# Kernel optimization log

Measured on AMD Instinct MI355X. Metric: run time of the kernel, lower is better.

## Reference

```python
import jax, jax.numpy as jnp
import numpy as np

Q_R = jnp.array([-1.0 / np.sqrt(2.0), 1.0 / np.sqrt(2.0)], dtype=jnp.float32)
N_U, N_H, N_MLP, N_CONV, N_Q = 8, 12, 16, 2, 2


def setup_inputs() -> dict:
    B, n = 16, 1024
    key = jax.random.key(0)
    ks = jax.random.split(key, 24)
    lin_w = lambda k, o, i: (jax.random.normal(k, (o, i), jnp.float32) * 0.1)
    lin_b = lambda k, o: (jax.random.normal(k, (o,), jnp.float32) * 0.1)
    inp = {
        "y": jax.random.normal(ks[0], (B, n), jnp.float32),
        "H": jax.random.normal(ks[1], (B, n, n), jnp.float32),
        "r": jax.random.normal(ks[2], (B, n), jnp.float32),
        "nu_r": jax.random.uniform(ks[3], (B, n), jnp.float32),
        "adj": (jax.random.uniform(ks[4], (B, n, n)) < 0.05).astype(jnp.float32),
        # W1: Linear(2, n_u) plus extra bias b1
        "W1_w": lin_w(ks[5], N_U, 2), "W1_b": lin_b(ks[6], N_U),
        "b1": jnp.zeros((N_U,), jnp.float32),
        # msg_mlp: Linear(3*n_u, n_mlp_hidden) -> ReLU -> Linear(n_mlp_hidden, n_u)
        "Wm1_w": lin_w(ks[7], N_MLP, 3 * N_U), "Wm1_b": lin_b(ks[8], N_MLP),
        "Wm2_w": lin_w(ks[9], N_U, N_MLP), "Wm2_b": lin_b(ks[10], N_U),
        # GRUCell(n_u + 2, n_h); gate order: r, z, n
        "gru_w_ih": lin_w(ks[11], 3 * N_H, N_U + 2), "gru_w_hh": lin_w(ks[12], 3 * N_H, N_H),
        "gru_b_ih": lin_b(ks[13], 3 * N_H), "gru_b_hh": lin_b(ks[14], 3 * N_H),
        # W2: Linear(n_h, n_u) plus extra bias b2
        "W2_w": lin_w(ks[15], N_U, N_H), "W2_b": lin_b(ks[16], N_U),
        "b2": jnp.zeros((N_U,), jnp.float32),
        # readout: Linear(n_u, n_mlp_hidden) -> ReLU -> Linear(n_mlp_hidden, N_Q)
        "Wr1_w": lin_w(ks[17], N_MLP, N_U), "Wr1_b": lin_b(ks[18], N_MLP),
        "Wr2_w": lin_w(ks[19], N_Q, N_MLP), "Wr2_b": lin_b(ks[20], N_Q),
    }
    return inp


def reference(y, H, r, nu_r, adj, W1_w, W1_b, b1, Wm1_w, Wm1_b, Wm2_w, Wm2_b,
              gru_w_ih, gru_w_hh, gru_b_ih, gru_b_hh, W2_w, W2_b, b2,
              Wr1_w, Wr1_b, Wr2_w, Wr2_b):
    B, n = y.shape
    yh = jnp.einsum('bi,bij->bj', y, H)          # (B,n)
    hh = jnp.sum(H * H, axis=1)                  # (B,n), column norms
    feat = jnp.stack([yh, hh], axis=-1)          # (B,n,2)
    u = feat @ W1_w.T + W1_b + b1                # (B,n,n_u)
    G = jnp.einsum('bki,bkj->bij', H, H)         # H^T H, (B,n,n)
    a_i = jnp.stack([r, jnp.maximum(nu_r, 1e-10)], axis=-1)  # (B,n,2)

    # masked-sum aggregation, fused (same math as expand+cat+mask+sum):
    #   agg = [u_i * deg_i, sum_j adj_ij u_j, (sum_j adj_ij G_ij) * 1_{n_u}]
    deg = jnp.sum(adj, axis=2)                   # (B,n)
    eg = jnp.sum(adj * G, axis=2)                # (B,n)
    eg_part = jnp.repeat(eg[..., None], N_U, axis=-1)  # (B,n,n_u)

    s = jnp.zeros((B, n, N_H), dtype=y.dtype)
    for _ in range(N_CONV):
        agg = jnp.concatenate([
            u * deg[..., None],
            jnp.einsum('bij,bjd->bid', adj, u),
            eg_part,
        ], axis=-1)                              # (B,n,3*n_u)
        m = jax.nn.relu(agg @ Wm1_w.T + Wm1_b) @ Wm2_w.T + Wm2_b  # (B,n,n_u)
        x = jnp.concatenate([m, a_i], axis=-1)   # (B,n,n_u+2)
        gx = x @ gru_w_ih.T + gru_b_ih
        gh = s @ gru_w_hh.T + gru_b_hh
        xr, xz, xn = jnp.split(gx, 3, axis=-1)
        hr, hz, hn = jnp.split(gh, 3, axis=-1)
        rg = jax.nn.sigmoid(xr + hr)
        zg = jax.nn.sigmoid(xz + hz)
        ng = jnp.tanh(xn + rg * hn)
        s = (1.0 - zg) * ng + zg * s             # (B,n,n_h)
        u = s @ W2_w.T + W2_b + b2               # (B,n,n_u)

    logits = jax.nn.relu(u @ Wr1_w.T + Wr1_b) @ Wr2_w.T + Wr2_b  # (B,n,N_Q)
    p = jax.nn.softmax(logits, axis=-1)
    x_hat = jnp.sum(p * Q_R, axis=-1)            # (B,n)
    nu_x = jnp.sum(p * (Q_R - x_hat[..., None]) ** 2, axis=-1)
    nu_x = jnp.maximum(nu_x, 1e-10)
    return (x_hat, nu_x)
```

## Files before the change

kernel.cpp:

```cpp
#include <hip/hip_runtime.h>

#define NB 16
#define NN 1024
#define NBN (NB * NN)
#define MAXN 128
#define NU 8
#define NH 12
#define NMLP 16
#define KC 16
#define NCHUNK (NN / KC)

#define QSW(j, c) (((j) << 4) + ((((c) ^ (((j) >> 2) & 3)) & 3) << 2))

__global__ __launch_bounds__(256) void k_build_idx(
    const float* __restrict__ adj, unsigned short* __restrict__ idxT,
    int* __restrict__ cnt, float* __restrict__ deg,
    float* __restrict__ eg, float* __restrict__ yhh) {
  const int row = blockIdx.x * 4 + (threadIdx.x >> 6);
  const int lane = threadIdx.x & 63;
  const float4* arow = (const float4*)(adj + (size_t)row * NN);
  float4 v[4];
#pragma unroll
  for (int rep = 0; rep < 4; ++rep) v[rep] = arow[rep * 64 + lane];
  const unsigned long long ltmask = (1ull << lane) - 1ull;
  int base = 0;
#pragma unroll
  for (int rep = 0; rep < 4; ++rep) {
    float c[4] = {v[rep].x, v[rep].y, v[rep].z, v[rep].w};
#pragma unroll
    for (int cc = 0; cc < 4; ++cc) {
      bool nz = (c[cc] != 0.0f);
      unsigned long long m = __ballot(nz);
      if (nz) {
        int p = base + __popcll(m & ltmask);
        if (p < MAXN)
          idxT[(size_t)p * NBN + row] = (unsigned short)(rep * 256 + lane * 4 + cc);
      }
      base += __popcll(m);
    }
  }
  if (lane == 0) {
    cnt[row] = base < MAXN ? base : MAXN;
    deg[row] = (float)base;
    eg[row] = 0.f; yhh[2 * row] = 0.f; yhh[2 * row + 1] = 0.f;
  }
}

__global__ __launch_bounds__(512) void k_eg(
    const float* __restrict__ H, const float* __restrict__ y,
    const unsigned short* __restrict__ idxT, const int* __restrict__ cnt,
    float* __restrict__ eg, float* __restrict__ yhh) {
  __shared__ float hsT[NN * KC];
  const int b = blockIdx.x >> 6;
  const int k0 = (blockIdx.x & 63) * KC;
  const int tid = threadIdx.x;
  const float* Hb = H + ((size_t)b * NN + k0) * NN;

  for (int j0 = tid; j0 < NN; j0 += 512) {
    float hv[KC];
#pragma unroll
    for (int k = 0; k < KC; ++k) hv[k] = Hb[(size_t)k * NN + j0];
#pragma unroll
    for (int c = 0; c < 4; ++c)
      *(float4*)&hsT[QSW(j0, c)] = ((const float4*)hv)[c];
  }
  __syncthreads();

  {
    float yv[KC];
#pragma unroll
    for (int k = 0; k < KC; ++k) yv[k] = y[b * NN + k0 + k];
    for (int j = tid; j < NN; j += 512) {
      float hv[KC];
#pragma unroll
      for (int c = 0; c < 4; ++c)
        ((float4*)hv)[c] = *(const float4*)&hsT[QSW(j, c)];
      float py = 0.f, ph = 0.f;
#pragma unroll
      for (int k = 0; k < KC; ++k) { py += yv[k] * hv[k]; ph += hv[k] * hv[k]; }
      atomicAdd(&yhh[(b * NN + j) * 2], py);
      atomicAdd(&yhh[(b * NN + j) * 2 + 1], ph);
    }
  }

  for (int rep = 0; rep < 2; ++rep) {
    const int i = rep * 512 + tid;
    const int node = b * NN + i;
    const int nnz = cnt[node];
    float hi[KC];
#pragma unroll
    for (int c = 0; c < 4; ++c)
      ((float4*)hi)[c] = *(const float4*)&hsT[QSW(i, c)];
    float a0 = 0.f, a1 = 0.f, a2 = 0.f, a3 = 0.f;
#pragma unroll 2
    for (int t = 0; t < nnz; ++t) {
      const int j = (int)idxT[(size_t)t * NBN + node];
      float hj[KC];
#pragma unroll
      for (int c = 0; c < 4; ++c)
        ((float4*)hj)[c] = *(const float4*)&hsT[QSW(j, c)];
#pragma unroll
      for (int k = 0; k < 4; ++k) {
        a0 += hi[k] * hj[k];
        a1 += hi[4 + k] * hj[4 + k];
        a2 += hi[8 + k] * hj[8 + k];
        a3 += hi[12 + k] * hj[12 + k];
      }
    }
    atomicAdd(&eg[node], (a0 + a1) + (a2 + a3));
  }
}

template <int PHASE>
__global__ __launch_bounds__(64) void k_iter(
    const float* __restrict__ u_in, const float2* __restrict__ yhh,
    const unsigned short* __restrict__ idxT, const int* __restrict__ cnt,
    const float* __restrict__ deg, const float* __restrict__ eg,
    const float* __restrict__ rin, const float* __restrict__ nur,
    const float* __restrict__ W1w, const float* __restrict__ W1b,
    const float* __restrict__ b1,
    const float* __restrict__ Wm1w, const float* __restrict__ Wm1b,
    const float* __restrict__ Wm2w, const float* __restrict__ Wm2b,
    const float* __restrict__ gih, const float* __restrict__ ghh,
    const float* __restrict__ bih, const float* __restrict__ bhh,
    const float* __restrict__ W2w, const float* __restrict__ W2b,
    const float* __restrict__ b2,
    const float* __restrict__ Wr1w, const float* __restrict__ Wr1b,
    const float* __restrict__ Wr2w, const float* __restrict__ Wr2b,
    float* __restrict__ s, float* __restrict__ u_out, float* __restrict__ out) {
  __shared__ float sWm1[NMLP * 3 * NU], sWm1b[NMLP], sWm2[NU * NMLP], sWm2b[NU];
  __shared__ float sgih[36 * (NU + 2)], sghh[36 * NH], sbih[36], sbhh[36];
  __shared__ float sW2[NU * NH], sW2b[NU], sb2[NU];
  __shared__ float sWr1[NMLP * NU], sWr1b[NMLP], sWr2[2 * NMLP], sWr2b[2];
  __shared__ float sW1[2 * NU], sWb1[NU];
  {
    auto cp = [&](float* d, const float* so, int n) {
      for (int t = threadIdx.x; t < n; t += 64) d[t] = so[t];
    };
    cp(sWm1, Wm1w, NMLP * 3 * NU); cp(sWm1b, Wm1b, NMLP);
    cp(sWm2, Wm2w, NU * NMLP);     cp(sWm2b, Wm2b, NU);
    cp(sgih, gih, 36 * (NU + 2));
    cp(sbih, bih, 36);             cp(sbhh, bhh, 36);
    cp(sW2, W2w, NU * NH);         cp(sW2b, W2b, NU);   cp(sb2, b2, NU);
    if (PHASE == 1) {
      cp(sW1, W1w, 2 * NU);
      for (int t = threadIdx.x; t < NU; t += 64) sWb1[t] = W1b[t] + b1[t];
    } else {
      cp(sghh, ghh, 36 * NH);
      cp(sWr1, Wr1w, NMLP * NU);   cp(sWr1b, Wr1b, NMLP);
      cp(sWr2, Wr2w, 2 * NMLP);    cp(sWr2b, Wr2b, 2);
    }
  }
  __syncthreads();
  const int node = blockIdx.x * 64 + threadIdx.x;
  const int nnz = cnt[node];
  const int bbase = node & ~(NN - 1);

  float uself[NU], msv[NU];
  if (PHASE == 1) {
    float sy = 0.f, sh = 0.f;
#pragma unroll 4
    for (int t = 0; t < nnz; ++t) {
      const int j = (int)idxT[(size_t)t * NBN + node];
      float2 v = yhh[bbase + j];
      sy += v.x; sh += v.y;
    }
    const float2 w0 = yhh[node];
    const float fn = (float)nnz;
#pragma unroll
    for (int o = 0; o < NU; ++o) {
      uself[o] = w0.x * sW1[2 * o] + w0.y * sW1[2 * o + 1] + sWb1[o];
      msv[o] = sy * sW1[2 * o] + sh * sW1[2 * o + 1] + fn * sWb1[o];
    }
  } else {
    float4 acc0 = {0, 0, 0, 0}, acc1 = {0, 0, 0, 0};
#pragma unroll 4
    for (int t = 0; t < nnz; ++t) {
      const int j = (int)idxT[(size_t)t * NBN + node];
      const float4* up = (const float4*)(u_in + ((size_t)bbase + j) * NU);
      float4 a = up[0], c4 = up[1];
      acc0.x += a.x;  acc0.y += a.y;  acc0.z += a.z;  acc0.w += a.w;
      acc1.x += c4.x; acc1.y += c4.y; acc1.z += c4.z; acc1.w += c4.w;
    }
    msv[0] = acc0.x; msv[1] = acc0.y; msv[2] = acc0.z; msv[3] = acc0.w;
    msv[4] = acc1.x; msv[5] = acc1.y; msv[6] = acc1.z; msv[7] = acc1.w;
    const float4* up = (const float4*)(u_in + (size_t)node * NU);
    float4 a = up[0], c4 = up[1];
    uself[0] = a.x;  uself[1] = a.y;  uself[2] = a.z;  uself[3] = a.w;
    uself[4] = c4.x; uself[5] = c4.y; uself[6] = c4.z; uself[7] = c4.w;
  }

  float agg[3 * NU];
  const float d = deg[node], e = eg[node];
#pragma unroll
  for (int o = 0; o < NU; ++o) {
    agg[o] = uself[o] * d;
    agg[NU + o] = msv[o];
    agg[2 * NU + o] = e;
  }
  float h1[NMLP];
#pragma unroll
  for (int h = 0; h < NMLP; ++h) {
    float t = sWm1b[h];
#pragma unroll
    for (int i = 0; i < 3 * NU; ++i) t += sWm1[h * 3 * NU + i] * agg[i];
    h1[h] = fmaxf(t, 0.f);
  }
  float x[NU + 2];
#pragma unroll
  for (int o = 0; o < NU; ++o) {
    float t = sWm2b[o];
#pragma unroll
    for (int h = 0; h < NMLP; ++h) t += sWm2[o * NMLP + h] * h1[h];
    x[o] = t;
  }
  x[NU] = rin[node];
  x[NU + 1] = fmaxf(nur[node], 1e-10f);

  float sv[NH];
#pragma unroll
  for (int g = 0; g < NH; ++g)
    sv[g] = (PHASE == 1) ? 0.f : s[(size_t)node * NH + g];

  float sn[NH];
#pragma unroll
  for (int g = 0; g < NH; ++g) {
    float xr = sbih[g], xz = sbih[NH + g], xn = sbih[2 * NH + g];
#pragma unroll
    for (int i = 0; i < NU + 2; ++i) {
      xr += sgih[g * (NU + 2) + i] * x[i];
      xz += sgih[(NH + g) * (NU + 2) + i] * x[i];
      xn += sgih[(2 * NH + g) * (NU + 2) + i] * x[i];
    }
    float hr = sbhh[g], hz = sbhh[NH + g], hn = sbhh[2 * NH + g];
    if (PHASE != 1) {
#pragma unroll
      for (int i = 0; i < NH; ++i) {
        hr += sghh[g * NH + i] * sv[i];
        hz += sghh[(NH + g) * NH + i] * sv[i];
        hn += sghh[(2 * NH + g) * NH + i] * sv[i];
      }
    }
    float rg = 1.f / (1.f + expf(-(xr + hr)));
    float zg = 1.f / (1.f + expf(-(xz + hz)));
    float ng = tanhf(xn + rg * hn);
    sn[g] = (1.f - zg) * ng + zg * sv[g];
  }

  if (PHASE == 1) {
#pragma unroll
    for (int g = 0; g < NH; ++g) s[(size_t)node * NH + g] = sn[g];
  }

  float un[NU];
#pragma unroll
  for (int o = 0; o < NU; ++o) {
    float t = sW2b[o] + sb2[o];
#pragma unroll
    for (int h = 0; h < NH; ++h) t += sW2[o * NH + h] * sn[h];
    un[o] = t;
  }
  if (PHASE == 1) {
#pragma unroll
    for (int o = 0; o < NU; ++o) u_out[(size_t)node * NU + o] = un[o];
  }

  if (PHASE == 2) {
    float h2[NMLP];
#pragma unroll
    for (int h = 0; h < NMLP; ++h) {
      float t = sWr1b[h];
#pragma unroll
      for (int o = 0; o < NU; ++o) t += sWr1[h * NU + o] * un[o];
      h2[h] = fmaxf(t, 0.f);
    }
    float l0 = sWr2b[0], l1 = sWr2b[1];
#pragma unroll
    for (int h = 0; h < NMLP; ++h) {
      l0 += sWr2[h] * h2[h];
      l1 += sWr2[NMLP + h] * h2[h];
    }
    float mx = fmaxf(l0, l1);
    float e0 = expf(l0 - mx), e1 = expf(l1 - mx);
    float inv = 1.f / (e0 + e1);
    float p0 = e0 * inv, p1 = e1 * inv;
    const float q0 = -0.70710678118654752f, q1 = 0.70710678118654752f;
    float xh = p0 * q0 + p1 * q1;
    float nu = p0 * (q0 - xh) * (q0 - xh) + p1 * (q1 - xh) * (q1 - xh);
    out[node] = xh;
    out[NB * NN + node] = fmaxf(nu, 1e-10f);
  }
}

extern "C" void kernel_launch(void* const* d_in, const int* in_sizes, int n_in,
                              void* d_out, int out_size, void* d_ws,
                              size_t ws_size, hipStream_t stream) {
  const float* y    = (const float*)d_in[0];
  const float* H    = (const float*)d_in[1];
  const float* r    = (const float*)d_in[2];
  const float* nur  = (const float*)d_in[3];
  const float* adj  = (const float*)d_in[4];
  const float* W1w  = (const float*)d_in[5];
  const float* W1b  = (const float*)d_in[6];
  const float* b1   = (const float*)d_in[7];
  const float* Wm1w = (const float*)d_in[8];
  const float* Wm1b = (const float*)d_in[9];
  const float* Wm2w = (const float*)d_in[10];
  const float* Wm2b = (const float*)d_in[11];
  const float* gih  = (const float*)d_in[12];
  const float* ghh  = (const float*)d_in[13];
  const float* bih  = (const float*)d_in[14];
  const float* bhh  = (const float*)d_in[15];
  const float* W2w  = (const float*)d_in[16];
  const float* W2b  = (const float*)d_in[17];
  const float* b2   = (const float*)d_in[18];
  const float* Wr1w = (const float*)d_in[19];
  const float* Wr1b = (const float*)d_in[20];
  const float* Wr2w = (const float*)d_in[21];
  const float* Wr2b = (const float*)d_in[22];
  float* out = (float*)d_out;

  char* p = (char*)d_ws;
  auto carve = [&](size_t bytes) {
    void* q = (void*)p;
    p += (bytes + 255) & ~(size_t)255;
    return q;
  };
  unsigned short* idxT = (unsigned short*)carve((size_t)MAXN * NBN * 2);
  int*   cnt  = (int*)  carve((size_t)NBN * 4);
  float* deg  = (float*)carve((size_t)NBN * 4);
  float* eg   = (float*)carve((size_t)NBN * 4);
  float* yhh  = (float*)carve((size_t)NBN * 8);
  float* u    = (float*)carve((size_t)NBN * NU * 4);
  float* s    = (float*)carve((size_t)NBN * NH * 4);

  k_build_idx<<<NBN / 4, 256, 0, stream>>>(adj, idxT, cnt, deg, eg, yhh);
  k_eg<<<NB * NCHUNK, 512, 0, stream>>>(H, y, idxT, cnt, eg, yhh);

  k_iter<1><<<NBN / 64, 64, 0, stream>>>(
      u, (const float2*)yhh, idxT, cnt, deg, eg, r, nur, W1w, W1b, b1,
      Wm1w, Wm1b, Wm2w, Wm2b, gih, ghh, bih, bhh, W2w, W2b, b2,
      Wr1w, Wr1b, Wr2w, Wr2b, s, u, out);
  k_iter<2><<<NBN / 64, 64, 0, stream>>>(
      u, (const float2*)yhh, idxT, cnt, deg, eg, r, nur, W1w, W1b, b1,
      Wm1w, Wm1b, Wm2w, Wm2b, gih, ghh, bih, bhh, W2w, W2b, b2,
      Wr1w, Wr1b, Wr2w, Wr2b, s, u, out);
}
```

Before: 348.1 us.

## Fuse all stages into one cooperative persistent kernel with grid syncs

Replaces the four-kernel pipeline (index build, H gram/eg, two GNN iterations) with a single cooperative kernel of 256 blocks that uses grid-wide syncs between stages and keeps weights in shared memory. A fallback path with three kernels is added; its final kernel runs both GNN iterations per batch in one block and keeps u in LDS. The aim is to remove launch gaps and tail effects between short kernels. In exchange, the grid is fixed at 256 blocks with grid-sync overhead, which could leave the eg stage with less parallelism than before.

```diff
diff --git a/kernel.cpp b/kernel.cpp
--- a/kernel.cpp
+++ b/kernel.cpp
@@ -1,4 +1,7 @@
 #include <hip/hip_runtime.h>
+#include <hip/hip_cooperative_groups.h>
+
+namespace cg = cooperative_groups;
 
 #define NB 16
 #define NN 1024
@@ -8,17 +11,153 @@
 #define NH 12
 #define NMLP 16
 #define KC 16
-#define NCHUNK (NN / KC)
+#define EGB 512
+#define GRID2 256
+#define BLK 512
 
 #define QSW(j, c) (((j) << 4) + ((((c) ^ (((j) >> 2) & 3)) & 3) << 2))
-
-__global__ __launch_bounds__(256) void k_build_idx(
-    const float* __restrict__ adj, unsigned short* __restrict__ idxT,
-    int* __restrict__ cnt, float* __restrict__ deg,
-    float* __restrict__ eg, float* __restrict__ yhh) {
-  const int row = blockIdx.x * 4 + (threadIdx.x >> 6);
-  const int lane = threadIdx.x & 63;
-  const float4* arow = (const float4*)(adj + (size_t)row * NN);
+#define USW(j, c) (((j) << 3) + ((((c) ^ (((j) >> 2) & 1)) & 1) << 2))
+
+#define W_M1   0
+#define W_M1B  384
+#define W_M2   400
+#define W_M2B  528
+#define W_GIH  536
+#define W_GHH  896
+#define W_BIH  1328
+#define W_BHH  1364
+#define W_W2   1400
+#define W_W2B  1496
+#define W_R1   1504
+#define W_R1B  1632
+#define W_R2   1648
+#define W_R2B  1680
+#define W_W1   1682
+#define W_W1B  1698
+#define W_SZ   1712
+
+struct KParams {
+  const float *y, *H, *r, *nur, *adj;
+  const float *W1w, *W1b, *b1, *Wm1w, *Wm1b, *Wm2w, *Wm2b;
+  const float *gih, *ghh, *bih, *bhh, *W2w, *W2b, *b2;
+  const float *Wr1w, *Wr1b, *Wr2w, *Wr2b;
+  unsigned short* idxT;
+  int* cnt;
+  float *deg, *eg, *yhh, *u, *s, *out;
+};
+
+template <bool FIRST>
+__device__ __forceinline__ void mlp_gru(const float* __restrict__ sm,
+                                        const float* uself, const float* msv,
+                                        float d, float e, float xr9, float xn10,
+                                        const float* sv, float* sn, float* un) {
+  float agg[3 * NU];
+#pragma unroll
+  for (int o = 0; o < NU; ++o) {
+    agg[o] = uself[o] * d;
+    agg[NU + o] = msv[o];
+    agg[2 * NU + o] = e;
+  }
+  float h1[NMLP];
+#pragma unroll
+  for (int h = 0; h < NMLP; ++h) {
+    float t = sm[W_M1B + h];
+#pragma unroll
+    for (int i = 0; i < 3 * NU; ++i) t += sm[W_M1 + h * 3 * NU + i] * agg[i];
+    h1[h] = fmaxf(t, 0.f);
+  }
+  float x[NU + 2];
+#pragma unroll
+  for (int o = 0; o < NU; ++o) {
+    float t = sm[W_M2B + o];
+#pragma unroll
+    for (int h = 0; h < NMLP; ++h) t += sm[W_M2 + o * NMLP + h] * h1[h];
+    x[o] = t;
+  }
+  x[NU] = xr9;
+  x[NU + 1] = xn10;
+
+#pragma unroll
+  for (int g = 0; g < NH; ++g) {
+    float xr = sm[W_BIH + g], xz = sm[W_BIH + NH + g], xn = sm[W_BIH + 2 * NH + g];
+#pragma unroll
+    for (int i = 0; i < NU + 2; ++i) {
+      xr += sm[W_GIH + g * (NU + 2) + i] * x[i];
+      xz += sm[W_GIH + (NH + g) * (NU + 2) + i] * x[i];
+      xn += sm[W_GIH + (2 * NH + g) * (NU + 2) + i] * x[i];
+    }
+    float hr = sm[W_BHH + g], hz = sm[W_BHH + NH + g], hn = sm[W_BHH + 2 * NH + g];
+    if (!FIRST) {
+#pragma unroll
+      for (int i = 0; i < NH; ++i) {
+        hr += sm[W_GHH + g * NH + i] * sv[i];
+        hz += sm[W_GHH + (NH + g) * NH + i] * sv[i];
+        hn += sm[W_GHH + (2 * NH + g) * NH + i] * sv[i];
+      }
+    }
+    float rg = 1.f / (1.f + expf(-(xr + hr)));
+    float zg = 1.f / (1.f + expf(-(xz + hz)));
+    float ng = tanhf(xn + rg * hn);
+    sn[g] = FIRST ? (1.f - zg) * ng : ((1.f - zg) * ng + zg * sv[g]);
+  }
+#pragma unroll
+  for (int o = 0; o < NU; ++o) {
+    float t = sm[W_W2B + o];
+#pragma unroll
+    for (int h = 0; h < NH; ++h) t += sm[W_W2 + o * NH + h] * sn[h];
+    un[o] = t;
+  }
+}
+
+__device__ __forceinline__ void do_readout(const float* __restrict__ sm,
+                                           const float* un,
+                                           float* __restrict__ out, int node) {
+  float h2[NMLP];
+#pragma unroll
+  for (int h = 0; h < NMLP; ++h) {
+    float t = sm[W_R1B + h];
+#pragma unroll
+    for (int o = 0; o < NU; ++o) t += sm[W_R1 + h * NU + o] * un[o];
+    h2[h] = fmaxf(t, 0.f);
+  }
+  float l0 = sm[W_R2B], l1 = sm[W_R2B + 1];
+#pragma unroll
+  for (int h = 0; h < NMLP; ++h) {
+    l0 += sm[W_R2 + h] * h2[h];
+    l1 += sm[W_R2 + NMLP + h] * h2[h];
+  }
+  float mx = fmaxf(l0, l1);
+  float e0 = expf(l0 - mx), e1 = expf(l1 - mx);
+  float inv = 1.f / (e0 + e1);
+  float p0 = e0 * inv, p1 = e1 * inv;
+  const float q0 = -0.70710678118654752f, q1 = 0.70710678118654752f;
+  float xh = p0 * q0 + p1 * q1;
+  float nu = p0 * (q0 - xh) * (q0 - xh) + p1 * (q1 - xh) * (q1 - xh);
+  out[node] = xh;
+  out[NBN + node] = fmaxf(nu, 1e-10f);
+}
+
+__device__ __forceinline__ void stage_weights(const KParams& P, float* sm,
+                                              int tid, int nthr) {
+  auto cp = [&](int dst, const float* so, int n) {
+    for (int t = tid; t < n; t += nthr) sm[dst + t] = so[t];
+  };
+  cp(W_M1, P.Wm1w, NMLP * 3 * NU); cp(W_M1B, P.Wm1b, NMLP);
+  cp(W_M2, P.Wm2w, NU * NMLP);     cp(W_M2B, P.Wm2b, NU);
+  cp(W_GIH, P.gih, 36 * (NU + 2)); cp(W_GHH, P.ghh, 36 * NH);
+  cp(W_BIH, P.bih, 36);            cp(W_BHH, P.bhh, 36);
+  cp(W_W2, P.W2w, NU * NH);
+  cp(W_R1, P.Wr1w, NMLP * NU);     cp(W_R1B, P.Wr1b, NMLP);
+  cp(W_R2, P.Wr2w, 2 * NMLP);      cp(W_R2B, P.Wr2b, 2);
+  cp(W_W1, P.W1w, 2 * NU);
+  for (int t = tid; t < NU; t += nthr) {
+    sm[W_W2B + t] = P.W2b[t] + P.b2[t];
+    sm[W_W1B + t] = P.W1b[t] + P.b1[t];
+  }
+}
+
+__device__ __forceinline__ void build_row(const KParams& P, int row, int lane) {
+  const float4* arow = (const float4*)(P.adj + (size_t)row * NN);
   float4 v[4];
 #pragma unroll
   for (int rep = 0; rep < 4; ++rep) v[rep] = arow[rep * 64 + lane];
@@ -34,29 +173,28 @@
       if (nz) {
         int p = base + __popcll(m & ltmask);
         if (p < MAXN)
-          idxT[(size_t)p * NBN + row] = (unsigned short)(rep * 256 + lane * 4 + cc);
+          P.idxT[(size_t)p * NBN + row] =
+              (unsigned short)(rep * 256 + lane * 4 + cc);
       }
       base += __popcll(m);
     }
   }
   if (lane == 0) {
-    cnt[row] = base < MAXN ? base : MAXN;
-    deg[row] = (float)base;
-    eg[row] = 0.f; yhh[2 * row] = 0.f; yhh[2 * row + 1] = 0.f;
-  }
-}
-
-__global__ __launch_bounds__(512) void k_eg(
-    const float* __restrict__ H, const float* __restrict__ y,
-    const unsigned short* __restrict__ idxT, const int* __restrict__ cnt,
-    float* __restrict__ eg, float* __restrict__ yhh) {
-  __shared__ float hsT[NN * KC];
-  const int b = blockIdx.x >> 6;
-  const int k0 = (blockIdx.x & 63) * KC;
-  const int tid = threadIdx.x;
-  const float* Hb = H + ((size_t)b * NN + k0) * NN;
-
-  for (int j0 = tid; j0 < NN; j0 += 512) {
+    P.cnt[row] = base < MAXN ? base : MAXN;
+    P.deg[row] = (float)base;
+    P.eg[row] = 0.f;
+    P.yhh[2 * row] = 0.f;
+    P.yhh[2 * row + 1] = 0.f;
+  }
+}
+
+template <int NTHR>
+__device__ __forceinline__ void eg_tile(const KParams& P, float* hsT, int bc,
+                                        int tid) {
+  const int b = bc >> 6;
+  const int k0 = (bc & 63) * KC;
+  const float* Hb = P.H + ((size_t)b * NN + k0) * NN;
+  for (int j0 = tid; j0 < NN; j0 += NTHR) {
     float hv[KC];
 #pragma unroll
     for (int k = 0; k < KC; ++k) hv[k] = Hb[(size_t)k * NN + j0];
@@ -69,8 +207,8 @@
   {
     float yv[KC];
 #pragma unroll
-    for (int k = 0; k < KC; ++k) yv[k] = y[b * NN + k0 + k];
-    for (int j = tid; j < NN; j += 512) {
+    for (int k = 0; k < KC; ++k) yv[k] = P.y[b * NN + k0 + k];
+    for (int j = tid; j < NN; j += NTHR) {
       float hv[KC];
 #pragma unroll
       for (int c = 0; c < 4; ++c)
@@ -78,23 +216,24 @@
       float py = 0.f, ph = 0.f;
 #pragma unroll
       for (int k = 0; k < KC; ++k) { py += yv[k] * hv[k]; ph += hv[k] * hv[k]; }
-      atomicAdd(&yhh[(b * NN + j) * 2], py);
-      atomicAdd(&yhh[(b * NN + j) * 2 + 1], ph);
-    }
-  }
-
-  for (int rep = 0; rep < 2; ++rep) {
-    const int i = rep * 512 + tid;
+      atomicAdd(&P.yhh[(b * NN + j) * 2], py);
+      atomicAdd(&P.yhh[(b * NN + j) * 2 + 1], ph);
+    }
+  }
+
+  for (int rep = 0; rep < NN / NTHR; ++rep) {
+    const int i = rep * NTHR + tid;
     const int node = b * NN + i;
-    const int nnz = cnt[node];
+    const int nnz = P.cnt[node];
     float hi[KC];
 #pragma unroll
     for (int c = 0; c < 4; ++c)
       ((float4*)hi)[c] = *(const float4*)&hsT[QSW(i, c)];
     float a0 = 0.f, a1 = 0.f, a2 = 0.f, a3 = 0.f;
+    int off = node;
 #pragma unroll 2
     for (int t = 0; t < nnz; ++t) {
-      const int j = (int)idxT[(size_t)t * NBN + node];
+      const int j = (int)P.idxT[off]; off += NBN;
       float hj[KC];
 #pragma unroll
       for (int c = 0; c < 4; ++c)
@@ -107,219 +246,161 @@
         a3 += hi[12 + k] * hj[12 + k];
       }
     }
-    atomicAdd(&eg[node], (a0 + a1) + (a2 + a3));
-  }
-}
-
-template <int PHASE>
-__global__ __launch_bounds__(64) void k_iter(
-    const float* __restrict__ u_in, const float2* __restrict__ yhh,
-    const unsigned short* __restrict__ idxT, const int* __restrict__ cnt,
-    const float* __restrict__ deg, const float* __restrict__ eg,
-    const float* __restrict__ rin, const float* __restrict__ nur,
-    const float* __restrict__ W1w, const float* __restrict__ W1b,
-    const float* __restrict__ b1,
-    const float* __restrict__ Wm1w, const float* __restrict__ Wm1b,
-    const float* __restrict__ Wm2w, const float* __restrict__ Wm2b,
-    const float* __restrict__ gih, const float* __restrict__ ghh,
-    const float* __restrict__ bih, const float* __restrict__ bhh,
-    const float* __restrict__ W2w, const float* __restrict__ W2b,
-    const float* __restrict__ b2,
-    const float* __restrict__ Wr1w, const float* __restrict__ Wr1b,
-    const float* __restrict__ Wr2w, const float* __restrict__ Wr2b,
-    float* __restrict__ s, float* __restrict__ u_out, float* __restrict__ out) {
-  __shared__ float sWm1[NMLP * 3 * NU], sWm1b[NMLP], sWm2[NU * NMLP], sWm2b[NU];
-  __shared__ float sgih[36 * (NU + 2)], sghh[36 * NH], sbih[36], sbhh[36];
-  __shared__ float sW2[NU * NH], sW2b[NU], sb2[NU];
-  __shared__ float sWr1[NMLP * NU], sWr1b[NMLP], sWr2[2 * NMLP], sWr2b[2];
-  __shared__ float sW1[2 * NU], sWb1[NU];
+    atomicAdd(&P.eg[node], (a0 + a1) + (a2 + a3));
+  }
+}
+
+__global__ __launch_bounds__(256) void k_build_idx(KParams P) {
+  build_row(P, blockIdx.x * 4 + (threadIdx.x >> 6), threadIdx.x & 63);
+}
+
+__global__ __launch_bounds__(EGB) void k_eg(KParams P) {
+  __shared__ float hsT[NN * KC];
+  eg_tile<EGB>(P, hsT, blockIdx.x, threadIdx.x);
+}
+
+__global__ __launch_bounds__(NN, 4) void k_fin(KParams P) {
+  __shared__ float su[NN * NU];
+  __shared__ float sm[W_SZ];
+  const int tid = threadIdx.x, b = blockIdx.x;
+  stage_weights(P, sm, tid, NN);
+  __syncthreads();
+
+  const int node = b * NN + tid;
+  const int nnz = P.cnt[node];
+  const float d = P.deg[node], e = P.eg[node];
+  const float rr = P.r[node];
+  const float nu = fmaxf(P.nur[node], 1e-10f);
+
+  float sy = 0.f, sh = 0.f;
   {
-    auto cp = [&](float* d, const float* so, int n) {
-      for (int t = threadIdx.x; t < n; t += 64) d[t] = so[t];
-    };
-    cp(sWm1, Wm1w, NMLP * 3 * NU); cp(sWm1b, Wm1b, NMLP);
-    cp(sWm2, Wm2w, NU * NMLP);     cp(sWm2b, Wm2b, NU);
-    cp(sgih, gih, 36 * (NU + 2));
-    cp(sbih, bih, 36);             cp(sbhh, bhh, 36);
-    cp(sW2, W2w, NU * NH);         cp(sW2b, W2b, NU);   cp(sb2, b2, NU);
-    if (PHASE == 1) {
-      cp(sW1, W1w, 2 * NU);
-      for (int t = threadIdx.x; t < NU; t += 64) sWb1[t] = W1b[t] + b1[t];
-    } else {
-      cp(sghh, ghh, 36 * NH);
-      cp(sWr1, Wr1w, NMLP * NU);   cp(sWr1b, Wr1b, NMLP);
-      cp(sWr2, Wr2w, 2 * NMLP);    cp(sWr2b, Wr2b, 2);
-    }
-  }
-  __syncthreads();
-  const int node = blockIdx.x * 64 + threadIdx.x;
-  const int nnz = cnt[node];
-  const int bbase = node & ~(NN - 1);
-
-  float uself[NU], msv[NU];
-  if (PHASE == 1) {
-    float sy = 0.f, sh = 0.f;
+    int off = node;
 #pragma unroll 4
     for (int t = 0; t < nnz; ++t) {
-      const int j = (int)idxT[(size_t)t * NBN + node];
-      float2 v = yhh[bbase + j];
+      const int j = (int)P.idxT[off]; off += NBN;
+      float2 v = ((const float2*)P.yhh)[b * NN + j];
       sy += v.x; sh += v.y;
     }
-    const float2 w0 = yhh[node];
-    const float fn = (float)nnz;
-#pragma unroll
-    for (int o = 0; o < NU; ++o) {
-      uself[o] = w0.x * sW1[2 * o] + w0.y * sW1[2 * o + 1] + sWb1[o];
-      msv[o] = sy * sW1[2 * o] + sh * sW1[2 * o + 1] + fn * sWb1[o];
-    }
-  } else {
-    float4 acc0 = {0, 0, 0, 0}, acc1 = {0, 0, 0, 0};
+  }
+  const float2 w0 = ((const float2*)P.yhh)[node];
+  float uself[NU], msv[NU];
+  const float fn = (float)nnz;
+#pragma unroll
+  for (int o = 0; o < NU; ++o) {
+    const float wa = sm[W_W1 + 2 * o], wb = sm[W_W1 + 2 * o + 1];
+    const float bb = sm[W_W1B + o];
+    uself[o] = w0.x * wa + w0.y * wb + bb;
+    msv[o] = sy * wa + sh * wb + fn * bb;
+  }
+  float sv[NH], sn[NH], un[NU];
+  mlp_gru<true>(sm, uself, msv, d, e, rr, nu, sv, sn, un);
+
+#pragma unroll
+  for (int c = 0; c < 2; ++c) *(float4*)&su[USW(tid, c)] = ((float4*)un)[c];
+  __syncthreads();
+
+  float4 acc0 = {0, 0, 0, 0}, acc1 = {0, 0, 0, 0};
+  {
+    int off = node;
 #pragma unroll 4
     for (int t = 0; t < nnz; ++t) {
-      const int j = (int)idxT[(size_t)t * NBN + node];
-      const float4* up = (const float4*)(u_in + ((size_t)bbase + j) * NU);
+      const int j = (int)P.idxT[off]; off += NBN;
+      float4 a = *(const float4*)&su[USW(j, 0)];
+      float4 c4 = *(const float4*)&su[USW(j, 1)];
+      acc0.x += a.x;  acc0.y += a.y;  acc0.z += a.z;  acc0.w += a.w;
+      acc1.x += c4.x; acc1.y += c4.y; acc1.z += c4.z; acc1.w += c4.w;
+    }
+  }
+  msv[0] = acc0.x; msv[1] = acc0.y; msv[2] = acc0.z; msv[3] = acc0.w;
+  msv[4] = acc1.x; msv[5] = acc1.y; msv[6] = acc1.z; msv[7] = acc1.w;
+  float sn2[NH], un2[NU];
+  mlp_gru<false>(sm, un, msv, d, e, rr, nu, sn, sn2, un2);
+  do_readout(sm, un2, P.out, node);
+}
+
+__global__ __launch_bounds__(BLK, 2) void k_all(KParams P) {
+  __shared__ float smem[NN * KC];
+  cg::grid_group gg = cg::this_grid();
+  const int tid = threadIdx.x, bid = blockIdx.x;
+  const int wave = tid >> 6, lane = tid & 63;
+
+#pragma unroll
+  for (int rr = 0; rr < 8; ++rr)
+    build_row(P, bid * 64 + wave * 8 + rr, lane);
+  gg.sync();
+
+  for (int bc = bid; bc < NB * (NN / KC); bc += GRID2) {
+    __syncthreads();
+    eg_tile<BLK>(P, smem, bc, tid);
+  }
+  gg.sync();
+
+  stage_weights(P, smem, tid, BLK);
+  __syncthreads();
+
+  for (int node = bid * BLK + tid; node < NBN; node += GRID2 * BLK) {
+    const int nnz = P.cnt[node];
+    const int bb = node & ~(NN - 1);
+    float sy = 0.f, sh = 0.f;
+    int off = node;
+#pragma unroll 4
+    for (int t = 0; t < nnz; ++t) {
+      const int j = (int)P.idxT[off]; off += NBN;
+      float2 v = ((const float2*)P.yhh)[bb + j];
+      sy += v.x; sh += v.y;
+    }
+    const float2 w0 = ((const float2*)P.yhh)[node];
+    float uself[NU], msv[NU];
+    const float fn = (float)nnz;
+#pragma unroll
+    for (int o = 0; o < NU; ++o) {
+      const float wa = smem[W_W1 + 2 * o], wb = smem[W_W1 + 2 * o + 1];
+      const float bbv = smem[W_W1B + o];
+      uself[o] = w0.x * wa + w0.y * wb + bbv;
+      msv[o] = sy * wa + sh * wb + fn * bbv;
+    }
+    float sv[NH], sn[NH], un[NU];
+    mlp_gru<true>(smem, uself, msv, P.deg[node], P.eg[node], P.r[node],
+                  fmaxf(P.nur[node], 1e-10f), sv, sn, un);
+#pragma unroll
+    for (int g = 0; g < NH; ++g) P.s[(size_t)node * NH + g] = sn[g];
+#pragma unroll
+    for (int o = 0; o < NU; ++o) P.u[(size_t)node * NU + o] = un[o];
+  }
+  gg.sync();
+
+  for (int node = bid * BLK + tid; node < NBN; node += GRID2 * BLK) {
+    const int nnz = P.cnt[node];
+    const int bb = node & ~(NN - 1);
+    float4 acc0 = {0, 0, 0, 0}, acc1 = {0, 0, 0, 0};
+    int off = node;
+#pragma unroll 4
+    for (int t = 0; t < nnz; ++t) {
+      const int j = (int)P.idxT[off]; off += NBN;
+      const float4* up = (const float4*)(P.u + ((size_t)bb + j) * NU);
       float4 a = up[0], c4 = up[1];
       acc0.x += a.x;  acc0.y += a.y;  acc0.z += a.z;  acc0.w += a.w;
       acc1.x += c4.x; acc1.y += c4.y; acc1.z += c4.z; acc1.w += c4.w;
     }
+    float uself[NU], msv[NU];
     msv[0] = acc0.x; msv[1] = acc0.y; msv[2] = acc0.z; msv[3] = acc0.w;
     msv[4] = acc1.x; msv[5] = acc1.y; msv[6] = acc1.z; msv[7] = acc1.w;
-    const float4* up = (const float4*)(u_in + (size_t)node * NU);
+    const float4* up = (const float4*)(P.u + (size_t)node * NU);
     float4 a = up[0], c4 = up[1];
     uself[0] = a.x;  uself[1] = a.y;  uself[2] = a.z;  uself[3] = a.w;
     uself[4] = c4.x; uself[5] = c4.y; uself[6] = c4.z; uself[7] = c4.w;
-  }
-
-  float agg[3 * NU];
-  const float d = deg[node], e = eg[node];
-#pragma unroll
-  for (int o = 0; o < NU; ++o) {
-    agg[o] = uself[o] * d;
-    agg[NU + o] = msv[o];
-    agg[2 * NU + o] = e;
-  }
-  float h1[NMLP];
-#pragma unroll
-  for (int h = 0; h < NMLP; ++h) {
-    float t = sWm1b[h];
-#pragma unroll
-    for (int i = 0; i < 3 * NU; ++i) t += sWm1[h * 3 * NU + i] * agg[i];
-    h1[h] = fmaxf(t, 0.f);
-  }
-  float x[NU + 2];
-#pragma unroll
-  for (int o = 0; o < NU; ++o) {
-    float t = sWm2b[o];
-#pragma unroll
-    for (int h = 0; h < NMLP; ++h) t += sWm2[o * NMLP + h] * h1[h];
-    x[o] = t;
-  }
-  x[NU] = rin[node];
-  x[NU + 1] = fmaxf(nur[node], 1e-10f);
-
-  float sv[NH];
-#pragma unroll
-  for (int g = 0; g < NH; ++g)
-    sv[g] = (PHASE == 1) ? 0.f : s[(size_t)node * NH + g];
-
-  float sn[NH];
-#pragma unroll
-  for (int g = 0; g < NH; ++g) {
-    float xr = sbih[g], xz = sbih[NH + g], xn = sbih[2 * NH + g];
-#pragma unroll
-    for (int i = 0; i < NU + 2; ++i) {
-      xr += sgih[g * (NU + 2) + i] * x[i];
-      xz += sgih[(NH + g) * (NU + 2) + i] * x[i];
-      xn += sgih[(2 * NH + g) * (NU + 2) + i] * x[i];
-    }
-    float hr = sbhh[g], hz = sbhh[NH + g], hn = sbhh[2 * NH + g];
-    if (PHASE != 1) {
-#pragma unroll
-      for (int i = 0; i < NH; ++i) {
-        hr += sghh[g * NH + i] * sv[i];
-        hz += sghh[(NH + g) * NH + i] * sv[i];
-        hn += sghh[(2 * NH + g) * NH + i] * sv[i];
-      }
-    }
-    float rg = 1.f / (1.f + expf(-(xr + hr)));
-    float zg = 1.f / (1.f + expf(-(xz + hz)));
-    float ng = tanhf(xn + rg * hn);
-    sn[g] = (1.f - zg) * ng + zg * sv[g];
-  }
-
-  if (PHASE == 1) {
-#pragma unroll
-    for (int g = 0; g < NH; ++g) s[(size_t)node * NH + g] = sn[g];
-  }
-
-  float un[NU];
-#pragma unroll
-  for (int o = 0; o < NU; ++o) {
-    float t = sW2b[o] + sb2[o];
-#pragma unroll
-    for (int h = 0; h < NH; ++h) t += sW2[o * NH + h] * sn[h];
-    un[o] = t;
-  }
-  if (PHASE == 1) {
-#pragma unroll
-    for (int o = 0; o < NU; ++o) u_out[(size_t)node * NU + o] = un[o];
-  }
-
-  if (PHASE == 2) {
-    float h2[NMLP];
-#pragma unroll
-    for (int h = 0; h < NMLP; ++h) {
-      float t = sWr1b[h];
-#pragma unroll
-      for (int o = 0; o < NU; ++o) t += sWr1[h * NU + o] * un[o];
-      h2[h] = fmaxf(t, 0.f);
-    }
-    float l0 = sWr2b[0], l1 = sWr2b[1];
-#pragma unroll
-    for (int h = 0; h < NMLP; ++h) {
-      l0 += sWr2[h] * h2[h];
-      l1 += sWr2[NMLP + h] * h2[h];
-    }
-    float mx = fmaxf(l0, l1);
-    float e0 = expf(l0 - mx), e1 = expf(l1 - mx);
-    float inv = 1.f / (e0 + e1);
-    float p0 = e0 * inv, p1 = e1 * inv;
-    const float q0 = -0.70710678118654752f, q1 = 0.70710678118654752f;
-    float xh = p0 * q0 + p1 * q1;
-    float nu = p0 * (q0 - xh) * (q0 - xh) + p1 * (q1 - xh) * (q1 - xh);
-    out[node] = xh;
-    out[NB * NN + node] = fmaxf(nu, 1e-10f);
+    float sv[NH], sn[NH], un[NU];
+#pragma unroll
+    for (int g = 0; g < NH; ++g) sv[g] = P.s[(size_t)node * NH + g];
+    mlp_gru<false>(smem, uself, msv, P.deg[node], P.eg[node], P.r[node],
+                   fmaxf(P.nur[node], 1e-10f), sv, sn, un);
+    do_readout(smem, un, P.out, node);
   }
 }
 
 extern "C" void kernel_launch(void* const* d_in, const int* in_sizes, int n_in,
                               void* d_out, int out_size, void* d_ws,
                               size_t ws_size, hipStream_t stream) {
-  const float* y    = (const float*)d_in[0];
-  const float* H    = (const float*)d_in[1];
-  const float* r    = (const float*)d_in[2];
-  const float* nur  = (const float*)d_in[3];
-  const float* adj  = (const float*)d_in[4];
-  const float* W1w  = (const float*)d_in[5];
-  const float* W1b  = (const float*)d_in[6];
-  const float* b1   = (const float*)d_in[7];
-  const float* Wm1w = (const float*)d_in[8];
-  const float* Wm1b = (const float*)d_in[9];
-  const float* Wm2w = (const float*)d_in[10];
-  const float* Wm2b = (const float*)d_in[11];
-  const float* gih  = (const float*)d_in[12];
-  const float* ghh  = (const float*)d_in[13];
-  const float* bih  = (const float*)d_in[14];
-  const float* bhh  = (const float*)d_in[15];
-  const float* W2w  = (const float*)d_in[16];
-  const float* W2b  = (const float*)d_in[17];
-  const float* b2   = (const float*)d_in[18];
-  const float* Wr1w = (const float*)d_in[19];
-  const float* Wr1b = (const float*)d_in[20];
-  const float* Wr2w = (const float*)d_in[21];
-  const float* Wr2b = (const float*)d_in[22];
-  float* out = (float*)d_out;
-
   char* p = (char*)d_ws;
   auto carve = [&](size_t bytes) {
     void* q = (void*)p;
@@ -327,22 +408,58 @@
     return q;
   };
   unsigned short* idxT = (unsigned short*)carve((size_t)MAXN * NBN * 2);
-  int*   cnt  = (int*)  carve((size_t)NBN * 4);
-  float* deg  = (float*)carve((size_t)NBN * 4);
-  float* eg   = (float*)carve((size_t)NBN * 4);
-  float* yhh  = (float*)carve((size_t)NBN * 8);
-  float* u    = (float*)carve((size_t)NBN * NU * 4);
-  float* s    = (float*)carve((size_t)NBN * NH * 4);
-
-  k_build_idx<<<NBN / 4, 256, 0, stream>>>(adj, idxT, cnt, deg, eg, yhh);
-  k_eg<<<NB * NCHUNK, 512, 0, stream>>>(H, y, idxT, cnt, eg, yhh);
-
-  k_iter<1><<<NBN / 64, 64, 0, stream>>>(
-      u, (const float2*)yhh, idxT, cnt, deg, eg, r, nur, W1w, W1b, b1,
-      Wm1w, Wm1b, Wm2w, Wm2b, gih, ghh, bih, bhh, W2w, W2b, b2,
-      Wr1w, Wr1b, Wr2w, Wr2b, s, u, out);
-  k_iter<2><<<NBN / 64, 64, 0, stream>>>(
-      u, (const float2*)yhh, idxT, cnt, deg, eg, r, nur, W1w, W1b, b1,
-      Wm1w, Wm1b, Wm2w, Wm2b, gih, ghh, bih, bhh, W2w, W2b, b2,
-      Wr1w, Wr1b, Wr2w, Wr2b, s, u, out);
-}
+  int*   cnt = (int*)  carve((size_t)NBN * 4);
+  float* deg = (float*)carve((size_t)NBN * 4);
+  float* eg  = (float*)carve((size_t)NBN * 4);
+  float* yhh = (float*)carve((size_t)NBN * 8);
+  float* u   = (float*)carve((size_t)NBN * NU * 4);
+  float* s   = (float*)carve((size_t)NBN * NH * 4);
+
+  KParams prm;
+  prm.y    = (const float*)d_in[0];
+  prm.H    = (const float*)d_in[1];
+  prm.r    = (const float*)d_in[2];
+  prm.nur  = (const float*)d_in[3];
+  prm.adj  = (const float*)d_in[4];
+  prm.W1w  = (const float*)d_in[5];
+  prm.W1b  = (const float*)d_in[6];
+  prm.b1   = (const float*)d_in[7];
+  prm.Wm1w = (const float*)d_in[8];
+  prm.Wm1b = (const float*)d_in[9];
+  prm.Wm2w = (const float*)d_in[10];
+  prm.Wm2b = (const float*)d_in[11];
+  prm.gih  = (const float*)d_in[12];
+  prm.ghh  = (const float*)d_in[13];
+  prm.bih  = (const float*)d_in[14];
+  prm.bhh  = (const float*)d_in[15];
+  prm.W2w  = (const float*)d_in[16];
+  prm.W2b  = (const float*)d_in[17];
+  prm.b2   = (const float*)d_in[18];
+  prm.Wr1w = (const float*)d_in[19];
+  prm.Wr1b = (const float*)d_in[20];
+  prm.Wr2w = (const float*)d_in[21];
+  prm.Wr2b = (const float*)d_in[22];
+  prm.idxT = idxT; prm.cnt = cnt; prm.deg = deg; prm.eg = eg;
+  prm.yhh = yhh; prm.u = u; prm.s = s;
+  prm.out = (float*)d_out;
+
+  int dev = 0;
+  (void)hipGetDevice(&dev);
+  int coop = 0, ncu = 0, maxb = 0;
+  (void)hipDeviceGetAttribute(&coop, hipDeviceAttributeCooperativeLaunch, dev);
+  (void)hipDeviceGetAttribute(&ncu, hipDeviceAttributeMultiprocessorCount, dev);
+  (void)hipOccupancyMaxActiveBlocksPerMultiprocessor(&maxb, k_all, BLK, 0);
+
+  hipError_t e = hipErrorUnknown;
+  if (coop && (size_t)maxb * (size_t)ncu >= GRID2) {
+    void* args[] = {(void*)&prm};
+    e = hipLaunchCooperativeKernel((void*)k_all, dim3(GRID2), dim3(BLK), args,
+                                   0, stream);
+  }
+  if (e != hipSuccess) {
+    (void)hipGetLastError();
+    k_build_idx<<<NBN / 4, 256, 0, stream>>>(prm);
+    k_eg<<<NB * (NN / KC), EGB, 0, stream>>>(prm);
+    k_fin<<<NB, NN, 0, stream>>>(prm);
+  }
+}
```

New measurement: 443.4 us. +27.4%, slower.
